# Performance work log

Hardware: AMD Instinct MI355X
Metric: run time of the kernel (lower is better)

## Reference

```python
import jax, jax.numpy as jnp
import numpy as np

E, C = 50000, 128  # edges, out_channels (heads=1 so H*C == C)
EPS = 1e-5

def _ln(x, g, b):
    m = x.mean(-1, keepdims=True)
    v = x.var(-1, keepdims=True)
    return (x - m) / jnp.sqrt(v + EPS) * g + b

def _mlp(x, W1, b1, W2, b2):
    return jax.nn.silu(x @ W1 + b1) @ W2 + b2

def setup_inputs() -> dict:
    key = jax.random.key(0)
    ks = jax.random.split(key, 32)
    s = 0.02
    d = {}
    d['edge'] = jax.random.normal(ks[0], (E, C), jnp.float32)
    d['edge_nei_len'] = jax.random.normal(ks[1], (E, 3, C), jnp.float32)
    d['edge_nei_angle'] = jax.random.normal(ks[2], (E, 3, C), jnp.float32)
    # lin_query / lin_key / lin_value (C -> H*C == C)
    d['Wq'] = jax.random.normal(ks[3], (C, C), jnp.float32) * s
    d['bq'] = jnp.zeros((C,), jnp.float32)
    d['Wk'] = jax.random.normal(ks[4], (C, C), jnp.float32) * s
    d['bk'] = jnp.zeros((C,), jnp.float32)
    d['Wv'] = jax.random.normal(ks[5], (C, C), jnp.float32) * s
    d['bv'] = jnp.zeros((C,), jnp.float32)
    # lin_key_e1/e2/e3 and lin_value_e1/e2/e3 stacked along first axis (3 lattice dirs)
    d['Wke'] = jax.random.normal(ks[6], (3, C, C), jnp.float32) * s
    d['bke'] = jnp.zeros((3, C), jnp.float32)
    d['Wve'] = jax.random.normal(ks[7], (3, C, C), jnp.float32) * s
    d['bve'] = jnp.zeros((3, C), jnp.float32)
    # lin_edge (no bias)
    d['We'] = jax.random.normal(ks[8], (C, C), jnp.float32) * s
    # lin_concate
    d['Wc'] = jax.random.normal(ks[9], (C, C), jnp.float32) * s
    d['bc'] = jnp.zeros((C,), jnp.float32)
    # key_update MLP: 3C -> C -> C
    d['Wk1'] = jax.random.normal(ks[10], (3 * C, C), jnp.float32) * s
    d['bk1'] = jnp.zeros((C,), jnp.float32)
    d['Wk2'] = jax.random.normal(ks[11], (C, C), jnp.float32) * s
    d['bk2'] = jnp.zeros((C,), jnp.float32)
    # lin_msg_update MLP: 3C -> C -> C
    d['Wm1'] = jax.random.normal(ks[12], (3 * C, C), jnp.float32) * s
    d['bm1'] = jnp.zeros((C,), jnp.float32)
    d['Wm2'] = jax.random.normal(ks[13], (C, C), jnp.float32) * s
    d['bm2'] = jnp.zeros((C,), jnp.float32)
    # LayerNorms
    d['g_att'] = jnp.ones((C,), jnp.float32)
    d['b_att'] = jnp.zeros((C,), jnp.float32)
    d['g_bn'] = jnp.ones((C,), jnp.float32)
    d['b_bn'] = jnp.zeros((C,), jnp.float32)
    return d

def reference(edge, edge_nei_len, edge_nei_angle,
              Wq, bq, Wk, bk, Wv, bv,
              Wke, bke, Wve, bve, We, Wc, bc,
              Wk1, bk1, Wk2, bk2, Wm1, bm1, Wm2, bm2,
              g_att, b_att, g_bn, b_bn):
    # per-edge projections, broadcast over the 3 lattice directions (repeat in torch)
    q = (edge @ Wq + bq)[:, None, :]           # [E,1,C]
    kx = (edge @ Wk + bk)[:, None, :]          # [E,1,C]
    vx = (edge @ Wv + bv)[:, None, :]          # [E,1,C]
    kx3 = jnp.broadcast_to(kx, (edge.shape[0], 3, kx.shape[-1]))
    vx3 = jnp.broadcast_to(vx, (edge.shape[0], 3, vx.shape[-1]))
    # per-direction projections of lattice embedding (lin_key_e1..3 / lin_value_e1..3)
    ky = jnp.einsum('eti,tio->eto', edge_nei_len, Wke) + bke   # [E,3,C]
    vy = jnp.einsum('eti,tio->eto', edge_nei_len, Wve) + bve   # [E,3,C]
    exy = edge_nei_angle @ We                                   # [E,3,C]
    # key_update MLP and attention score
    k = _mlp(jnp.concatenate([kx3, ky, exy], axis=-1), Wk1, bk1, Wk2, bk2)  # [E,3,C]
    alpha = q * k / jnp.sqrt(jnp.float32(k.shape[-1]))
    # message MLP, sigmoid gate on LayerNorm'd alpha
    msg = _mlp(jnp.concatenate([vx3, vy, exy], axis=-1), Wm1, bm1, Wm2, bm2)
    out = msg * jax.nn.sigmoid(_ln(alpha, g_att, b_att))
    out = out @ Wc + bc        # lin_concate (H*C -> C)
    out = out.sum(axis=1)      # sum over 3 directions -> [E,C]
    return jax.nn.softplus(edge + _ln(out, g_bn, b_bn))
```

## Files before the change

kernel.cpp:

```cpp
#include <hip/hip_runtime.h>

#define E_TOTAL 50000
#define NTILES  3125

#define OFF_WSB 458752ull
#define OFF_Q   524288ull
#define OFF_EK  (OFF_Q  + 12800000ull)
#define OFF_EM  (OFF_EK + 12800000ull)
#define OFF_SK  (OFF_EM + 12800000ull)
#define OFF_SM  (OFF_SK + 38400000ull)
#define OFF_P2  (OFF_SM + 38400000ull)
#define WS_NEED (OFF_P2 + 12800000ull)

typedef float f4  __attribute__((ext_vector_type(4)));
typedef short s8v __attribute__((ext_vector_type(8)));
typedef short s4v __attribute__((ext_vector_type(4)));

typedef __attribute__((address_space(3))) unsigned lds_u32;
typedef __attribute__((address_space(1))) const unsigned g_u32;

__device__ __forceinline__ short f2bf(float x){
  unsigned u = __builtin_bit_cast(unsigned, x);
  u += 0x7fffu + ((u >> 16) & 1u);
  return (short)(u >> 16);
}
__device__ __forceinline__ float bf2f(short s){
  unsigned u = ((unsigned)(unsigned short)s) << 16;
  return __builtin_bit_cast(float, u);
}
__device__ __forceinline__ float sigm(float x){ return 1.f/(1.f + __expf(-x)); }

__device__ __forceinline__ s8v load_bfrag(const float* p){
  f4 a = *(const f4*)p;
  f4 b = *(const f4*)(p + 4);
  s8v r;
  r[0]=f2bf(a[0]); r[1]=f2bf(a[1]); r[2]=f2bf(a[2]); r[3]=f2bf(a[3]);
  r[4]=f2bf(b[0]); r[5]=f2bf(b[1]); r[6]=f2bf(b[2]); r[7]=f2bf(b[3]);
  return r;
}

__device__ __forceinline__ void mm8l(f4* acc, const s8v* B, const s8v* A, int lane){
  #pragma unroll
  for (int mb = 0; mb < 8; ++mb){
    #pragma unroll
    for (int kk = 0; kk < 4; ++kk){
      s8v af = A[(mb*4 + kk)*64 + lane];
      acc[mb] = __builtin_amdgcn_mfma_f32_16x16x32_bf16(af, B[kk], acc[mb], 0, 0, 0);
    }
  }
}

__device__ __forceinline__ void mm8f(f4* acc, const s8v* B, const s8v* A, int lane){
  #pragma unroll
  for (int mb = 0; mb < 8; mb += 2){
    #pragma unroll
    for (int m2 = 0; m2 < 2; ++m2){
      #pragma unroll
      for (int kk = 0; kk < 4; ++kk){
        s8v af = A[((mb+m2)*4 + kk)*64 + lane];
        acc[mb+m2] = __builtin_amdgcn_mfma_f32_16x16x32_bf16(af, B[kk], acc[mb+m2], 0, 0, 0);
      }
    }
    __builtin_amdgcn_sched_barrier(0);
  }
}

__device__ __forceinline__ void stage_mat(const short* __restrict__ src,
                                          short* dst, int wid, int lane){
  #pragma unroll
  for (int j = 0; j < 8; ++j){
    const short* gsrc = src + j*2048 + wid*512 + lane*8;
    short* ldst = dst + j*2048 + wid*512;
    __builtin_amdgcn_global_load_lds((g_u32*)(const void*)gsrc, (lds_u32*)(void*)ldst, 16, 0, 0);
  }
}

__device__ __forceinline__ s8v pack_pair(const f4& a0, const f4& a1){
  s8v o;
  #pragma unroll
  for (int p = 0; p < 4; ++p){ o[p] = f2bf(a0[p]); o[4+p] = f2bf(a1[p]); }
  return o;
}

__global__ __launch_bounds__(256) void pack_weights(
    const float* __restrict__ Wq, const float* __restrict__ Wk, const float* __restrict__ Wv,
    const float* __restrict__ Wke, const float* __restrict__ Wve, const float* __restrict__ We,
    const float* __restrict__ Wc, const float* __restrict__ Wk1, const float* __restrict__ Wk2,
    const float* __restrict__ Wm1, const float* __restrict__ Wm2,
    short* __restrict__ wsm)
{
  int mi   = blockIdx.x >> 6;
  int elem = ((blockIdx.x & 63) << 8) + threadIdx.x;
  int p  = elem & 7;
  int l  = (elem >> 3) & 63;
  int kk = (elem >> 9) & 3;
  int mb = elem >> 11;
  int gg = l >> 4;
  int m  = mb*16 + (l & 15);
  bool dlay = (mi == 5) || (mi == 6) || (mi == 7);
  int k = dlay ? (kk*32 + ((p < 4) ? (gg*4 + p) : (16 + gg*4 + (p - 4))))
               : (kk*32 + gg*8 + p);

  const float* X = nullptr; const float* Y = nullptr; const float* W = nullptr;
  switch (mi){
    case 0: W = Wq; break;
    case 1: X = Wk; Y = Wk1;            break;
    case 2: X = Wv; Y = Wm1;            break;
    case 3: X = We; Y = Wk1 + 256*128;  break;
    case 4: X = We; Y = Wm1 + 256*128;  break;
    case 5: W = Wk2; break;
    case 6: W = Wm2; break;
    case 7: W = Wc;  break;
    default:
      if (mi < 11){ X = Wke + (mi-8)*16384;  Y = Wk1 + 128*128; }
      else        { X = Wve + (mi-11)*16384; Y = Wm1 + 128*128; }
  }
  float v;
  if (W){
    v = W[k*128 + m];
  } else {
    v = 0.f;
    for (int j = 0; j < 128; ++j) v += X[k*128 + j] * Y[j*128 + m];
  }
  wsm[(size_t)mi*16384 + elem] = f2bf(v);
}

__global__ __launch_bounds__(128) void make_biases(
    const float* __restrict__ bk,  const float* __restrict__ bke, const float* __restrict__ bk1,
    const float* __restrict__ bv,  const float* __restrict__ bve, const float* __restrict__ bm1,
    const float* __restrict__ Wk1, const float* __restrict__ Wm1,
    float* __restrict__ wsb)
{
  int b = blockIdx.x;
  int t = b % 3;
  bool isM = b >= 3;
  int o = threadIdx.x;
  const float* W  = isM ? Wm1 : Wk1;
  const float* b0 = isM ? bv  : bk;
  const float* be = (isM ? bve : bke) + t*128;
  const float* b1 = isM ? bm1 : bk1;
  float v = b1[o];
  for (int j = 0; j < 128; ++j)
    v += b0[j]*W[j*128 + o] + be[j]*W[(128 + j)*128 + o];
  wsb[b*128 + o] = v;
}

__global__ __launch_bounds__(256) void proj(
    const float* __restrict__ edge, const float* __restrict__ bq,
    const short* __restrict__ wsm, char* __restrict__ ws)
{
  __shared__ short lds[3*16384];
  const int lane = threadIdx.x & 63;
  const int wid  = threadIdx.x >> 6;
  stage_mat(wsm + 0*16384, lds,          wid, lane);
  stage_mat(wsm + 1*16384, lds + 16384,  wid, lane);
  stage_mat(wsm + 2*16384, lds + 32768,  wid, lane);
  __syncthreads();
  const int g = lane >> 4, er = lane & 15;
  short* wq  = (short*)(ws + OFF_Q);
  short* wek = (short*)(ws + OFF_EK);
  short* wem = (short*)(ws + OFF_EM);

  #pragma unroll 1
  for (int tile = blockIdx.x*4 + wid; tile < NTILES; tile += 1024){
    const float* erow = edge + ((size_t)tile*16 + er)*128;
    s8v BE[4];
    #pragma unroll
    for (int kk = 0; kk < 4; ++kk) BE[kk] = load_bfrag(erow + kk*32 + g*8);

    f4 acc[8];
    #pragma unroll
    for (int mb = 0; mb < 8; ++mb) acc[mb] = *(const f4*)(bq + mb*16 + g*4);
    mm8f(acc, BE, (const s8v*)lds, lane);
    #pragma unroll
    for (int c = 0; c < 4; ++c)
      *(s8v*)(wq + (size_t)tile*2048 + c*512 + lane*8) = pack_pair(acc[2*c], acc[2*c+1]);

    #pragma unroll
    for (int mb = 0; mb < 8; ++mb){ f4 z = {0.f,0.f,0.f,0.f}; acc[mb] = z; }
    mm8f(acc, BE, (const s8v*)(lds + 16384), lane);
    #pragma unroll
    for (int c = 0; c < 4; ++c)
      *(s8v*)(wek + (size_t)tile*2048 + c*512 + lane*8) = pack_pair(acc[2*c], acc[2*c+1]);

    #pragma unroll
    for (int mb = 0; mb < 8; ++mb){ f4 z = {0.f,0.f,0.f,0.f}; acc[mb] = z; }
    mm8f(acc, BE, (const s8v*)(lds + 32768), lane);
    #pragma unroll
    for (int c = 0; c < 4; ++c)
      *(s8v*)(wem + (size_t)tile*2048 + c*512 + lane*8) = pack_pair(acc[2*c], acc[2*c+1]);
  }
}

__global__ __launch_bounds__(256) void hpass(
    const float* __restrict__ nlen, const float* __restrict__ nang,
    const short* __restrict__ wsm, const float* __restrict__ wsb,
    char* __restrict__ ws)
{
  __shared__ short lds[4*16384];
  const int lane = threadIdx.x & 63;
  const int wid  = threadIdx.x >> 6;
  const int t    = blockIdx.y;
  stage_mat(wsm + (size_t)(8 + t)*16384,  lds,         wid, lane);
  stage_mat(wsm + 3*16384,                lds + 16384, wid, lane);
  stage_mat(wsm + (size_t)(11 + t)*16384, lds + 32768, wid, lane);
  stage_mat(wsm + 4*16384,                lds + 49152, wid, lane);
  __syncthreads();
  const int g = lane >> 4, er = lane & 15;
  const float* biasK = wsb + t*128;
  const float* biasM = wsb + 384 + t*128;
  const short* wek = (const short*)(ws + OFF_EK);
  const short* wem = (const short*)(ws + OFF_EM);
  short* wsk  = (short*)(ws + OFF_SK + (size_t)t*12800000ull);
  short* wsm2 = (short*)(ws + OFF_SM + (size_t)t*12800000ull);

  #pragma unroll 1
  for (int tile = blockIdx.x*4 + wid; tile < NTILES; tile += 1024){
    const size_t e = (size_t)tile*16 + er;
    const float* lrow = nlen + (e*3 + t)*128;
    const float* arow = nang + (e*3 + t)*128;
    s8v BL[4], BA[4];
    #pragma unroll
    for (int kk = 0; kk < 4; ++kk){
      BL[kk] = load_bfrag(lrow + kk*32 + g*8);
      BA[kk] = load_bfrag(arow + kk*32 + g*8);
    }
    f4 acc[8];
    #pragma unroll
    for (int c = 0; c < 4; ++c){
      s8v ek8 = *(const s8v*)(wek + (size_t)tile*2048 + c*512 + lane*8);
      f4 b0 = *(const f4*)(biasK + (2*c)*16 + g*4);
      f4 b1 = *(const f4*)(biasK + (2*c+1)*16 + g*4);
      #pragma unroll
      for (int r = 0; r < 4; ++r){ b0[r] += bf2f(ek8[r]); b1[r] += bf2f(ek8[4+r]); }
      acc[2*c] = b0; acc[2*c+1] = b1;
    }
    mm8f(acc, BL, (const s8v*)lds, lane);
    mm8f(acc, BA, (const s8v*)(lds + 16384), lane);
    #pragma unroll
    for (int kk = 0; kk < 4; ++kk){
      s8v S;
      #pragma unroll
      for (int p = 0; p < 4; ++p){
        float x0 = acc[2*kk][p];   S[p]   = f2bf(x0 * sigm(x0));
        float x1 = acc[2*kk+1][p]; S[4+p] = f2bf(x1 * sigm(x1));
      }
      *(s8v*)(wsk + (size_t)tile*2048 + kk*512 + lane*8) = S;
    }
    #pragma unroll
    for (int c = 0; c < 4; ++c){
      s8v em8 = *(const s8v*)(wem + (size_t)tile*2048 + c*512 + lane*8);
      f4 b0 = *(const f4*)(biasM + (2*c)*16 + g*4);
      f4 b1 = *(const f4*)(biasM + (2*c+1)*16 + g*4);
      #pragma unroll
      for (int r = 0; r < 4; ++r){ b0[r] += bf2f(em8[r]); b1[r] += bf2f(em8[4+r]); }
      acc[2*c] = b0; acc[2*c+1] = b1;
    }
    mm8f(acc, BL, (const s8v*)(lds + 32768), lane);
    mm8f(acc, BA, (const s8v*)(lds + 49152), lane);
    #pragma unroll
    for (int kk = 0; kk < 4; ++kk){
      s8v S;
      #pragma unroll
      for (int p = 0; p < 4; ++p){
        float x0 = acc[2*kk][p];   S[p]   = f2bf(x0 * sigm(x0));
        float x1 = acc[2*kk+1][p]; S[4+p] = f2bf(x1 * sigm(x1));
      }
      *(s8v*)(wsm2 + (size_t)tile*2048 + kk*512 + lane*8) = S;
    }
  }
}

__global__ __launch_bounds__(256) void gpass(
    const float* __restrict__ bk2,  const float* __restrict__ bm2,
    const float* __restrict__ g_att, const float* __restrict__ b_att,
    const short* __restrict__ wsm, char* __restrict__ ws)
{
  __shared__ short lds[2*16384];
  const int lane = threadIdx.x & 63;
  const int wid  = threadIdx.x >> 6;
  const int t    = blockIdx.y;
  stage_mat(wsm + 5*16384, lds,         wid, lane);
  stage_mat(wsm + 6*16384, lds + 16384, wid, lane);
  __syncthreads();
  const int g = lane >> 4;
  const short* wq  = (const short*)(ws + OFF_Q);
  const short* wsk = (const short*)(ws + OFF_SK + (size_t)t*12800000ull);
  const short* wsm2= (const short*)(ws + OFF_SM + (size_t)t*12800000ull);
  const size_t poff[3] = {OFF_EK, OFF_EM, OFF_P2};
  short* wp = (short*)(ws + poff[t]);

  #pragma unroll 1
  for (int tile = blockIdx.x*4 + wid; tile < NTILES; tile += 1024){
    s8v SF[4];
    #pragma unroll
    for (int kk = 0; kk < 4; ++kk)
      SF[kk] = *(const s8v*)(wsk + (size_t)tile*2048 + kk*512 + lane*8);
    f4 acc[8];
    #pragma unroll
    for (int mb = 0; mb < 8; ++mb) acc[mb] = *(const f4*)(bk2 + mb*16 + g*4);
    mm8f(acc, SF, (const s8v*)lds, lane);

    float sm = 0.f, ssq = 0.f;
    #pragma unroll
    for (int c = 0; c < 4; ++c){
      s8v q8 = *(const s8v*)(wq + (size_t)tile*2048 + c*512 + lane*8);
      #pragma unroll
      for (int r = 0; r < 4; ++r){
        float a = bf2f(q8[r])   * acc[2*c][r]   * 0.08838834764831845f;
        float b = bf2f(q8[4+r]) * acc[2*c+1][r] * 0.08838834764831845f;
        acc[2*c][r] = a; acc[2*c+1][r] = b;
        sm += a + b; ssq += a*a + b*b;
      }
    }
    sm  += __shfl_xor(sm, 16);  sm  += __shfl_xor(sm, 32);
    ssq += __shfl_xor(ssq, 16); ssq += __shfl_xor(ssq, 32);
    float mean = sm * (1.f/128.f);
    float rstd = rsqrtf(ssq * (1.f/128.f) - mean*mean + 1e-5f);
    s4v gateb[8];
    #pragma unroll
    for (int mb = 0; mb < 8; ++mb){
      f4 ga = *(const f4*)(g_att + mb*16 + g*4);
      f4 bb = *(const f4*)(b_att + mb*16 + g*4);
      s4v t4;
      #pragma unroll
      for (int r = 0; r < 4; ++r)
        t4[r] = f2bf(sigm((acc[mb][r] - mean)*rstd*ga[r] + bb[r]));
      gateb[mb] = t4;
    }

    #pragma unroll
    for (int kk = 0; kk < 4; ++kk)
      SF[kk] = *(const s8v*)(wsm2 + (size_t)tile*2048 + kk*512 + lane*8);
    #pragma unroll
    for (int mb = 0; mb < 8; ++mb) acc[mb] = *(const f4*)(bm2 + mb*16 + g*4);
    mm8f(acc, SF, (const s8v*)(lds + 16384), lane);
    #pragma unroll
    for (int c = 0; c < 4; ++c){
      s8v o;
      #pragma unroll
      for (int p = 0; p < 4; ++p){
        o[p]   = f2bf(acc[2*c][p]   * bf2f(gateb[2*c][p]));
        o[4+p] = f2bf(acc[2*c+1][p] * bf2f(gateb[2*c+1][p]));
      }
      *(s8v*)(wp + (size_t)tile*2048 + c*512 + lane*8) = o;
    }
  }
}

__global__ __launch_bounds__(256) void fin(
    const float* __restrict__ edge, const float* __restrict__ bc,
    const float* __restrict__ g_bn, const float* __restrict__ b_bn,
    const short* __restrict__ wsm, const char* __restrict__ ws,
    float* __restrict__ out)
{
  __shared__ short lds[16384];
  const int lane = threadIdx.x & 63;
  const int wid  = threadIdx.x >> 6;
  stage_mat(wsm + 7*16384, lds, wid, lane);
  __syncthreads();
  const int g = lane >> 4, er = lane & 15;
  const short* p0 = (const short*)(ws + OFF_EK);
  const short* p1 = (const short*)(ws + OFF_EM);
  const short* p2 = (const short*)(ws + OFF_P2);

  #pragma unroll 1
  for (int tile = blockIdx.x*4 + wid; tile < NTILES; tile += 784){
    const size_t e = (size_t)tile*16 + er;
    const float* erow = edge + e*128;

    s8v GF[4];
    #pragma unroll
    for (int c = 0; c < 4; ++c){
      size_t idx = (size_t)tile*2048 + c*512 + lane*8;
      s8v a = *(const s8v*)(p0 + idx);
      s8v b = *(const s8v*)(p1 + idx);
      s8v d = *(const s8v*)(p2 + idx);
      s8v o;
      #pragma unroll
      for (int i = 0; i < 8; ++i) o[i] = f2bf(bf2f(a[i]) + bf2f(b[i]) + bf2f(d[i]));
      GF[c] = o;
    }
    f4 acc[8];
    #pragma unroll
    for (int mb = 0; mb < 8; ++mb){
      f4 b = *(const f4*)(bc + mb*16 + g*4);
      #pragma unroll
      for (int r = 0; r < 4; ++r) b[r] *= 3.f;
      acc[mb] = b;
    }
    mm8f(acc, GF, (const s8v*)lds, lane);

    float sm = 0.f, ssq = 0.f;
    #pragma unroll
    for (int mb = 0; mb < 8; ++mb){
      #pragma unroll
      for (int r = 0; r < 4; ++r){ sm += acc[mb][r]; ssq += acc[mb][r]*acc[mb][r]; }
    }
    sm  += __shfl_xor(sm, 16);  sm  += __shfl_xor(sm, 32);
    ssq += __shfl_xor(ssq, 16); ssq += __shfl_xor(ssq, 32);
    float mean = sm * (1.f/128.f);
    float rstd = rsqrtf(ssq * (1.f/128.f) - mean*mean + 1e-5f);

    #pragma unroll
    for (int mb = 0; mb < 8; ++mb){
      f4 ev  = *(const f4*)(erow + mb*16 + g*4);
      f4 gv  = *(const f4*)(g_bn + mb*16 + g*4);
      f4 bv2 = *(const f4*)(b_bn + mb*16 + g*4);
      f4 o;
      #pragma unroll
      for (int r = 0; r < 4; ++r){
        float x = ev[r] + (acc[mb][r] - mean)*rstd*gv[r] + bv2[r];
        o[r] = (x > 20.f) ? x : __logf(1.f + __expf(x));
      }
      *(f4*)(out + e*128 + mb*16 + g*4) = o;
    }
  }
}

__global__ __launch_bounds__(256) void edge_fused(
    const float* __restrict__ edge, const float* __restrict__ nlen, const float* __restrict__ nang,
    const float* __restrict__ bq,   const float* __restrict__ bk2,  const float* __restrict__ bm2,
    const float* __restrict__ bc,
    const float* __restrict__ g_att, const float* __restrict__ b_att,
    const float* __restrict__ g_bn,  const float* __restrict__ b_bn,
    const short* __restrict__ wsm,  const float* __restrict__ wsb,
    float* __restrict__ out)
{
  __shared__ short smem[2*16384];
  const int lane = threadIdx.x & 63;
  const int wid  = threadIdx.x >> 6;
  int tile = blockIdx.x*4 + wid;
  if (tile > NTILES-1) tile = NTILES-1;
  const int g  = lane >> 4;
  const int er = lane & 15;
  const size_t e = (size_t)tile*16 + er;
  const float* erow = edge + e*128;

  stage_mat(wsm + 0*16384, smem, wid, lane);
  s8v BE[4];
  #pragma unroll
  for (int kk = 0; kk < 4; ++kk) BE[kk] = load_bfrag(erow + kk*32 + g*8);
  f4 acc[8], gm[8];
  s4v qb[8], ekb[8], emb[8], gateb[8];
  s8v S[4], BL[4], BA[4];
  #pragma unroll
  for (int mb = 0; mb < 8; ++mb){ f4 z = {0.f,0.f,0.f,0.f}; gm[mb] = z; }
  __syncthreads();

  stage_mat(wsm + 1*16384, smem + 16384, wid, lane);
  #pragma unroll
  for (int mb = 0; mb < 8; ++mb) acc[mb] = *(const f4*)(bq + mb*16 + g*4);
  mm8l(acc, BE, (const s8v*)smem, lane);
  #pragma unroll
  for (int mb = 0; mb < 8; ++mb){
    s4v t4; t4[0]=f2bf(acc[mb][0]); t4[1]=f2bf(acc[mb][1]); t4[2]=f2bf(acc[mb][2]); t4[3]=f2bf(acc[mb][3]);
    qb[mb] = t4;
  }
  __syncthreads();

  stage_mat(wsm + 2*16384, smem, wid, lane);
  #pragma unroll
  for (int mb = 0; mb < 8; ++mb){ f4 z = {0.f,0.f,0.f,0.f}; acc[mb] = z; }
  mm8l(acc, BE, (const s8v*)(smem + 16384), lane);
  #pragma unroll
  for (int mb = 0; mb < 8; ++mb){
    s4v t4; t4[0]=f2bf(acc[mb][0]); t4[1]=f2bf(acc[mb][1]); t4[2]=f2bf(acc[mb][2]); t4[3]=f2bf(acc[mb][3]);
    ekb[mb] = t4;
  }
  __syncthreads();

  stage_mat(wsm + 8*16384, smem + 16384, wid, lane);
  #pragma unroll
  for (int mb = 0; mb < 8; ++mb){ f4 z = {0.f,0.f,0.f,0.f}; acc[mb] = z; }
  mm8l(acc, BE, (const s8v*)smem, lane);
  #pragma unroll
  for (int mb = 0; mb < 8; ++mb){
    s4v t4; t4[0]=f2bf(acc[mb][0]); t4[1]=f2bf(acc[mb][1]); t4[2]=f2bf(acc[mb][2]); t4[3]=f2bf(acc[mb][3]);
    emb[mb] = t4;
  }
  {
    const float* lrow = nlen + e*3*128;
    const float* arow = nang + e*3*128;
    #pragma unroll
    for (int kk = 0; kk < 4; ++kk){
      BL[kk] = load_bfrag(lrow + kk*32 + g*8);
      BA[kk] = load_bfrag(arow + kk*32 + g*8);
    }
  }
  __syncthreads();

  int cur = 1;
  #pragma unroll 1
  for (int t = 0; t < 3; ++t){
    stage_mat(wsm + 3*16384, smem + (cur^1)*16384, wid, lane);
    #pragma unroll
    for (int mb = 0; mb < 8; ++mb){
      f4 b = *(const f4*)(wsb + t*128 + mb*16 + g*4);
      #pragma unroll
      for (int r = 0; r < 4; ++r) b[r] += bf2f(ekb[mb][r]);
      acc[mb] = b;
    }
    mm8l(acc, BL, (const s8v*)(smem + cur*16384), lane);
    __syncthreads(); cur ^= 1;

    stage_mat(wsm + 5*16384, smem + (cur^1)*16384, wid, lane);
    mm8l(acc, BA, (const s8v*)(smem + cur*16384), lane);
    #pragma unroll
    for (int kk = 0; kk < 4; ++kk){
      #pragma unroll
      for (int p = 0; p < 4; ++p){
        float x0 = acc[2*kk][p];   S[kk][p]   = f2bf(x0 * sigm(x0));
        float x1 = acc[2*kk+1][p]; S[kk][4+p] = f2bf(x1 * sigm(x1));
      }
    }
    __syncthreads(); cur ^= 1;

    stage_mat(wsm + (size_t)(11+t)*16384, smem + (cur^1)*16384, wid, lane);
    #pragma unroll
    for (int mb = 0; mb < 8; ++mb) acc[mb] = *(const f4*)(bk2 + mb*16 + g*4);
    mm8l(acc, S, (const s8v*)(smem + cur*16384), lane);
    {
      float sm = 0.f, ssq = 0.f;
      #pragma unroll
      for (int mb = 0; mb < 8; ++mb){
        #pragma unroll
        for (int r = 0; r < 4; ++r){
          float a = bf2f(qb[mb][r]) * acc[mb][r] * 0.08838834764831845f;
          acc[mb][r] = a; sm += a; ssq += a*a;
        }
      }
      sm  += __shfl_xor(sm, 16);  sm  += __shfl_xor(sm, 32);
      ssq += __shfl_xor(ssq, 16); ssq += __shfl_xor(ssq, 32);
      float mean = sm * (1.f/128.f);
      float rstd = rsqrtf(ssq * (1.f/128.f) - mean*mean + 1e-5f);
      #pragma unroll
      for (int mb = 0; mb < 8; ++mb){
        f4 ga = *(const f4*)(g_att + mb*16 + g*4);
        f4 bb = *(const f4*)(b_att + mb*16 + g*4);
        s4v t4;
        #pragma unroll
        for (int r = 0; r < 4; ++r)
          t4[r] = f2bf(sigm((acc[mb][r] - mean)*rstd*ga[r] + bb[r]));
        gateb[mb] = t4;
      }
    }
    __syncthreads(); cur ^= 1;

    stage_mat(wsm + 4*16384, smem + (cur^1)*16384, wid, lane);
    #pragma unroll
    for (int mb = 0; mb < 8; ++mb){
      f4 b = *(const f4*)(wsb + 384 + t*128 + mb*16 + g*4);
      #pragma unroll
      for (int r = 0; r < 4; ++r) b[r] += bf2f(emb[mb][r]);
      acc[mb] = b;
    }
    mm8l(acc, BL, (const s8v*)(smem + cur*16384), lane);
    __syncthreads(); cur ^= 1;

    stage_mat(wsm + 6*16384, smem + (cur^1)*16384, wid, lane);
    mm8l(acc, BA, (const s8v*)(smem + cur*16384), lane);
    #pragma unroll
    for (int kk = 0; kk < 4; ++kk){
      #pragma unroll
      for (int p = 0; p < 4; ++p){
        float x0 = acc[2*kk][p];   S[kk][p]   = f2bf(x0 * sigm(x0));
        float x1 = acc[2*kk+1][p]; S[kk][4+p] = f2bf(x1 * sigm(x1));
      }
    }
    __syncthreads(); cur ^= 1;

    stage_mat(wsm + (size_t)(t < 2 ? 9 + t : 7)*16384, smem + (cur^1)*16384, wid, lane);
    #pragma unroll
    for (int mb = 0; mb < 8; ++mb) acc[mb] = *(const f4*)(bm2 + mb*16 + g*4);
    mm8l(acc, S, (const s8v*)(smem + cur*16384), lane);
    if (t < 2){
      const float* lrow = nlen + (e*3 + t + 1)*128;
      const float* arow = nang + (e*3 + t + 1)*128;
      #pragma unroll
      for (int kk = 0; kk < 4; ++kk){
        BL[kk] = load_bfrag(lrow + kk*32 + g*8);
        BA[kk] = load_bfrag(arow + kk*32 + g*8);
      }
    }
    #pragma unroll
    for (int mb = 0; mb < 8; ++mb){
      #pragma unroll
      for (int r = 0; r < 4; ++r) gm[mb][r] += acc[mb][r] * bf2f(gateb[mb][r]);
    }
    __syncthreads(); cur ^= 1;
  }

  s8v GF[4];
  #pragma unroll
  for (int kk = 0; kk < 4; ++kk){
    #pragma unroll
    for (int p = 0; p < 4; ++p){
      GF[kk][p]   = f2bf(gm[2*kk][p]);
      GF[kk][4+p] = f2bf(gm[2*kk+1][p]);
    }
  }
  #pragma unroll
  for (int mb = 0; mb < 8; ++mb){
    f4 b = *(const f4*)(bc + mb*16 + g*4);
    #pragma unroll
    for (int r = 0; r < 4; ++r) b[r] *= 3.f;
    acc[mb] = b;
  }
  mm8l(acc, GF, (const s8v*)(smem + cur*16384), lane);

  float sm = 0.f, ssq = 0.f;
  #pragma unroll
  for (int mb = 0; mb < 8; ++mb){
    #pragma unroll
    for (int r = 0; r < 4; ++r){ sm += acc[mb][r]; ssq += acc[mb][r]*acc[mb][r]; }
  }
  sm  += __shfl_xor(sm, 16);  sm  += __shfl_xor(sm, 32);
  ssq += __shfl_xor(ssq, 16); ssq += __shfl_xor(ssq, 32);
  float mean = sm * (1.f/128.f);
  float rstd = rsqrtf(ssq * (1.f/128.f) - mean*mean + 1e-5f);

  #pragma unroll
  for (int mb = 0; mb < 8; ++mb){
    f4 ev  = *(const f4*)(erow + mb*16 + g*4);
    f4 gv  = *(const f4*)(g_bn + mb*16 + g*4);
    f4 bv2 = *(const f4*)(b_bn + mb*16 + g*4);
    f4 o;
    #pragma unroll
    for (int r = 0; r < 4; ++r){
      float x = ev[r] + (acc[mb][r] - mean)*rstd*gv[r] + bv2[r];
      o[r] = (x > 20.f) ? x : log1pf(__expf(x));
    }
    *(f4*)(out + e*128 + mb*16 + g*4) = o;
  }
}

extern "C" void kernel_launch(void* const* d_in, const int* in_sizes, int n_in,
                              void* d_out, int out_size, void* d_ws, size_t ws_size,
                              hipStream_t stream)
{
  const float* edge = (const float*)d_in[0];
  const float* nlen = (const float*)d_in[1];
  const float* nang = (const float*)d_in[2];
  const float* Wq  = (const float*)d_in[3];
  const float* bq  = (const float*)d_in[4];
  const float* Wk  = (const float*)d_in[5];
  const float* bk  = (const float*)d_in[6];
  const float* Wv  = (const float*)d_in[7];
  const float* bv  = (const float*)d_in[8];
  const float* Wke = (const float*)d_in[9];
  const float* bke = (const float*)d_in[10];
  const float* Wve = (const float*)d_in[11];
  const float* bve = (const float*)d_in[12];
  const float* We  = (const float*)d_in[13];
  const float* Wc  = (const float*)d_in[14];
  const float* bc  = (const float*)d_in[15];
  const float* Wk1 = (const float*)d_in[16];
  const float* bk1 = (const float*)d_in[17];
  const float* Wk2 = (const float*)d_in[18];
  const float* bk2 = (const float*)d_in[19];
  const float* Wm1 = (const float*)d_in[20];
  const float* bm1 = (const float*)d_in[21];
  const float* Wm2 = (const float*)d_in[22];
  const float* bm2 = (const float*)d_in[23];
  const float* g_att = (const float*)d_in[24];
  const float* b_att = (const float*)d_in[25];
  const float* g_bn  = (const float*)d_in[26];
  const float* b_bn  = (const float*)d_in[27];

  short* wsm = (short*)d_ws;
  float* wsb = (float*)((char*)d_ws + OFF_WSB);
  char*  ws  = (char*)d_ws;

  pack_weights<<<dim3(14*64), dim3(256), 0, stream>>>(
      Wq, Wk, Wv, Wke, Wve, We, Wc, Wk1, Wk2, Wm1, Wm2, wsm);
  make_biases<<<dim3(6), dim3(128), 0, stream>>>(
      bk, bke, bk1, bv, bve, bm1, Wk1, Wm1, wsb);

  if (ws_size >= WS_NEED){
    proj<<<dim3(256), dim3(256), 0, stream>>>(edge, bq, wsm, ws);
    hpass<<<dim3(256, 3), dim3(256), 0, stream>>>(nlen, nang, wsm, wsb, ws);
    gpass<<<dim3(256, 3), dim3(256), 0, stream>>>(bk2, bm2, g_att, b_att, wsm, ws);
    fin<<<dim3(196), dim3(256), 0, stream>>>(
        edge, bc, g_bn, b_bn, wsm, ws, (float*)d_out);
  } else {
    edge_fused<<<dim3((NTILES + 3)/4), dim3(256), 0, stream>>>(
        edge, nlen, nang, bq, bk2, bm2, bc, g_att, b_att, g_bn, b_bn,
        wsm, wsb, (float*)d_out);
  }
}
```

Baseline: 198.9 us.

## Software-pipeline neighbour-feature loads with double-buffered registers in edge MLP pass

Splits the per-tile work into an issue phase that loads the fp32 lattice length/angle rows into registers and a compute phase that converts them to bf16 and runs the MFMA MLP. The loop is unrolled by two with ping-pong register buffers, so the global loads for the next tile are in flight while the current tile computes. This hides global-memory latency at the cost of 128 extra VGPRs per thread for the two buffers, which may reduce occupancy or cause spills.

```diff
diff --git a/kernel.cpp b/kernel.cpp
--- a/kernel.cpp
+++ b/kernel.cpp
@@ -214,16 +214,32 @@
   short* wsk  = (short*)(ws + OFF_SK + (size_t)t*12800000ull);
   short* wsm2 = (short*)(ws + OFF_SM + (size_t)t*12800000ull);
 
-  #pragma unroll 1
-  for (int tile = blockIdx.x*4 + wid; tile < NTILES; tile += 1024){
+  f4 rA[16], rB[16];
+
+  auto issue = [&](int tile, f4* r){
     const size_t e = (size_t)tile*16 + er;
     const float* lrow = nlen + (e*3 + t)*128;
     const float* arow = nang + (e*3 + t)*128;
+    #pragma unroll
+    for (int kk = 0; kk < 4; ++kk){
+      r[2*kk]     = *(const f4*)(lrow + kk*32 + g*8);
+      r[2*kk+1]   = *(const f4*)(lrow + kk*32 + g*8 + 4);
+      r[8+2*kk]   = *(const f4*)(arow + kk*32 + g*8);
+      r[8+2*kk+1] = *(const f4*)(arow + kk*32 + g*8 + 4);
+    }
+  };
+
+  auto doTile = [&](int tile, const f4* r){
     s8v BL[4], BA[4];
     #pragma unroll
     for (int kk = 0; kk < 4; ++kk){
-      BL[kk] = load_bfrag(lrow + kk*32 + g*8);
-      BA[kk] = load_bfrag(arow + kk*32 + g*8);
+      s8v bl, ba;
+      #pragma unroll
+      for (int p = 0; p < 4; ++p){
+        bl[p] = f2bf(r[2*kk][p]);     bl[4+p] = f2bf(r[2*kk+1][p]);
+        ba[p] = f2bf(r[8+2*kk][p]);   ba[4+p] = f2bf(r[8+2*kk+1][p]);
+      }
+      BL[kk] = bl; BA[kk] = ba;
     }
     f4 acc[8];
     #pragma unroll
@@ -232,7 +248,7 @@
       f4 b0 = *(const f4*)(biasK + (2*c)*16 + g*4);
       f4 b1 = *(const f4*)(biasK + (2*c+1)*16 + g*4);
       #pragma unroll
-      for (int r = 0; r < 4; ++r){ b0[r] += bf2f(ek8[r]); b1[r] += bf2f(ek8[4+r]); }
+      for (int rr = 0; rr < 4; ++rr){ b0[rr] += bf2f(ek8[rr]); b1[rr] += bf2f(ek8[4+rr]); }
       acc[2*c] = b0; acc[2*c+1] = b1;
     }
     mm8f(acc, BL, (const s8v*)lds, lane);
@@ -253,7 +269,7 @@
       f4 b0 = *(const f4*)(biasM + (2*c)*16 + g*4);
       f4 b1 = *(const f4*)(biasM + (2*c+1)*16 + g*4);
       #pragma unroll
-      for (int r = 0; r < 4; ++r){ b0[r] += bf2f(em8[r]); b1[r] += bf2f(em8[4+r]); }
+      for (int rr = 0; rr < 4; ++rr){ b0[rr] += bf2f(em8[rr]); b1[rr] += bf2f(em8[4+rr]); }
       acc[2*c] = b0; acc[2*c+1] = b1;
     }
     mm8f(acc, BL, (const s8v*)(lds + 32768), lane);
@@ -268,6 +284,18 @@
       }
       *(s8v*)(wsm2 + (size_t)tile*2048 + kk*512 + lane*8) = S;
     }
+  };
+
+  const int t0 = blockIdx.x*4 + wid;
+  issue(t0, rA);
+  #pragma unroll 1
+  for (int tile = t0; tile < NTILES; tile += 2048){
+    const int tn  = tile + 1024;
+    const int tnn = tile + 2048;
+    if (tn < NTILES) issue(tn, rB);
+    doTile(tile, rA);
+    if (tnn < NTILES) issue(tnn, rA);
+    if (tn < NTILES) doTile(tn, rB);
   }
 }
 
```

Result: slower. 212.5 us (+6.8%).

## Fuse gated-message pass with final projection and loop directions in-kernel

Applied to the files above, without the earlier changes.

Merges the per-direction gating pass and the final lin_concate/LayerNorm/softplus kernel into one kernel that loops over the three directions, accumulating the gated message in fp32 registers. This removes the writes and re-reads of three bf16 intermediate buffers and one kernel launch, and drops the extra workspace region. The hpass grid is also shrunk to 85x3 blocks with a matching stride. The fused kernel carries more registers and LDS (three staged matrices), which may reduce occupancy, and the 256 blocks now cover all three directions instead of 256 per direction.

```diff
diff --git a/kernel.cpp b/kernel.cpp
--- a/kernel.cpp
+++ b/kernel.cpp
@@ -9,8 +9,7 @@
 #define OFF_EM  (OFF_EK + 12800000ull)
 #define OFF_SK  (OFF_EM + 12800000ull)
 #define OFF_SM  (OFF_SK + 38400000ull)
-#define OFF_P2  (OFF_SM + 38400000ull)
-#define WS_NEED (OFF_P2 + 12800000ull)
+#define WS_NEED (OFF_SM + 38400000ull)
 
 typedef float f4  __attribute__((ext_vector_type(4)));
 typedef short s8v __attribute__((ext_vector_type(8)));
@@ -215,7 +214,7 @@
   short* wsm2 = (short*)(ws + OFF_SM + (size_t)t*12800000ull);
 
   #pragma unroll 1
-  for (int tile = blockIdx.x*4 + wid; tile < NTILES; tile += 1024){
+  for (int tile = blockIdx.x*4 + wid; tile < NTILES; tile += 340){
     const size_t e = (size_t)tile*16 + er;
     const float* lrow = nlen + (e*3 + t)*128;
     const float* arow = nang + (e*3 + t)*128;
@@ -271,137 +270,106 @@
   }
 }
 
-__global__ __launch_bounds__(256) void gpass(
+__global__ __launch_bounds__(256) void gfin(
+    const float* __restrict__ edge,
     const float* __restrict__ bk2,  const float* __restrict__ bm2,
+    const float* __restrict__ bc,
     const float* __restrict__ g_att, const float* __restrict__ b_att,
-    const short* __restrict__ wsm, char* __restrict__ ws)
+    const float* __restrict__ g_bn,  const float* __restrict__ b_bn,
+    const short* __restrict__ wsm, const char* __restrict__ ws,
+    float* __restrict__ out)
 {
-  __shared__ short lds[2*16384];
+  __shared__ short lds[3*16384];
   const int lane = threadIdx.x & 63;
   const int wid  = threadIdx.x >> 6;
-  const int t    = blockIdx.y;
   stage_mat(wsm + 5*16384, lds,         wid, lane);
   stage_mat(wsm + 6*16384, lds + 16384, wid, lane);
+  stage_mat(wsm + 7*16384, lds + 32768, wid, lane);
   __syncthreads();
-  const int g = lane >> 4;
-  const short* wq  = (const short*)(ws + OFF_Q);
-  const short* wsk = (const short*)(ws + OFF_SK + (size_t)t*12800000ull);
-  const short* wsm2= (const short*)(ws + OFF_SM + (size_t)t*12800000ull);
-  const size_t poff[3] = {OFF_EK, OFF_EM, OFF_P2};
-  short* wp = (short*)(ws + poff[t]);
+  const int g = lane >> 4, er = lane & 15;
+  const short* wq = (const short*)(ws + OFF_Q);
 
   #pragma unroll 1
   for (int tile = blockIdx.x*4 + wid; tile < NTILES; tile += 1024){
-    s8v SF[4];
-    #pragma unroll
-    for (int kk = 0; kk < 4; ++kk)
-      SF[kk] = *(const s8v*)(wsk + (size_t)tile*2048 + kk*512 + lane*8);
-    f4 acc[8];
-    #pragma unroll
-    for (int mb = 0; mb < 8; ++mb) acc[mb] = *(const f4*)(bk2 + mb*16 + g*4);
-    mm8f(acc, SF, (const s8v*)lds, lane);
+    const size_t e = (size_t)tile*16 + er;
+    f4 gm[8], acc[8], gate[8];
+    #pragma unroll
+    for (int mb = 0; mb < 8; ++mb){ f4 z = {0.f,0.f,0.f,0.f}; gm[mb] = z; }
+
+    #pragma unroll 1
+    for (int t = 0; t < 3; ++t){
+      const short* wsk  = (const short*)(ws + OFF_SK + (size_t)t*12800000ull);
+      const short* wsm2 = (const short*)(ws + OFF_SM + (size_t)t*12800000ull);
+      s8v SF[4];
+      #pragma unroll
+      for (int kk = 0; kk < 4; ++kk)
+        SF[kk] = *(const s8v*)(wsk + (size_t)tile*2048 + kk*512 + lane*8);
+      #pragma unroll
+      for (int mb = 0; mb < 8; ++mb) acc[mb] = *(const f4*)(bk2 + mb*16 + g*4);
+      mm8f(acc, SF, (const s8v*)lds, lane);
+
+      float sm = 0.f, ssq = 0.f;
+      #pragma unroll
+      for (int c = 0; c < 4; ++c){
+        s8v q8 = *(const s8v*)(wq + (size_t)tile*2048 + c*512 + lane*8);
+        #pragma unroll
+        for (int r = 0; r < 4; ++r){
+          float a = bf2f(q8[r])   * acc[2*c][r]   * 0.08838834764831845f;
+          float b = bf2f(q8[4+r]) * acc[2*c+1][r] * 0.08838834764831845f;
+          acc[2*c][r] = a; acc[2*c+1][r] = b;
+          sm += a + b; ssq += a*a + b*b;
+        }
+      }
+      sm  += __shfl_xor(sm, 16);  sm  += __shfl_xor(sm, 32);
+      ssq += __shfl_xor(ssq, 16); ssq += __shfl_xor(ssq, 32);
+      float mean = sm * (1.f/128.f);
+      float rstd = rsqrtf(ssq * (1.f/128.f) - mean*mean + 1e-5f);
+      #pragma unroll
+      for (int mb = 0; mb < 8; ++mb){
+        f4 ga = *(const f4*)(g_att + mb*16 + g*4);
+        f4 bb = *(const f4*)(b_att + mb*16 + g*4);
+        #pragma unroll
+        for (int r = 0; r < 4; ++r)
+          gate[mb][r] = sigm((acc[mb][r] - mean)*rstd*ga[r] + bb[r]);
+      }
+
+      #pragma unroll
+      for (int kk = 0; kk < 4; ++kk)
+        SF[kk] = *(const s8v*)(wsm2 + (size_t)tile*2048 + kk*512 + lane*8);
+      #pragma unroll
+      for (int mb = 0; mb < 8; ++mb) acc[mb] = *(const f4*)(bm2 + mb*16 + g*4);
+      mm8f(acc, SF, (const s8v*)(lds + 16384), lane);
+      #pragma unroll
+      for (int mb = 0; mb < 8; ++mb){
+        #pragma unroll
+        for (int r = 0; r < 4; ++r) gm[mb][r] += acc[mb][r] * gate[mb][r];
+      }
+    }
+
+    s8v GF[4];
+    #pragma unroll
+    for (int c = 0; c < 4; ++c) GF[c] = pack_pair(gm[2*c], gm[2*c+1]);
+    #pragma unroll
+    for (int mb = 0; mb < 8; ++mb){
+      f4 b = *(const f4*)(bc + mb*16 + g*4);
+      #pragma unroll
+      for (int r = 0; r < 4; ++r) b[r] *= 3.f;
+      acc[mb] = b;
+    }
+    mm8f(acc, GF, (const s8v*)(lds + 32768), lane);
 
     float sm = 0.f, ssq = 0.f;
     #pragma unroll
-    for (int c = 0; c < 4; ++c){
-      s8v q8 = *(const s8v*)(wq + (size_t)tile*2048 + c*512 + lane*8);
-      #pragma unroll
-      for (int r = 0; r < 4; ++r){
-        float a = bf2f(q8[r])   * acc[2*c][r]   * 0.08838834764831845f;
-        float b = bf2f(q8[4+r]) * acc[2*c+1][r] * 0.08838834764831845f;
-        acc[2*c][r] = a; acc[2*c+1][r] = b;
-        sm += a + b; ssq += a*a + b*b;
-      }
+    for (int mb = 0; mb < 8; ++mb){
+      #pragma unroll
+      for (int r = 0; r < 4; ++r){ sm += acc[mb][r]; ssq += acc[mb][r]*acc[mb][r]; }
     }
     sm  += __shfl_xor(sm, 16);  sm  += __shfl_xor(sm, 32);
     ssq += __shfl_xor(ssq, 16); ssq += __shfl_xor(ssq, 32);
     float mean = sm * (1.f/128.f);
     float rstd = rsqrtf(ssq * (1.f/128.f) - mean*mean + 1e-5f);
-    s4v gateb[8];
-    #pragma unroll
-    for (int mb = 0; mb < 8; ++mb){
-      f4 ga = *(const f4*)(g_att + mb*16 + g*4);
-      f4 bb = *(const f4*)(b_att + mb*16 + g*4);
-      s4v t4;
-      #pragma unroll
-      for (int r = 0; r < 4; ++r)
-        t4[r] = f2bf(sigm((acc[mb][r] - mean)*rstd*ga[r] + bb[r]));
-      gateb[mb] = t4;
-    }
-
-    #pragma unroll
-    for (int kk = 0; kk < 4; ++kk)
-      SF[kk] = *(const s8v*)(wsm2 + (size_t)tile*2048 + kk*512 + lane*8);
-    #pragma unroll
-    for (int mb = 0; mb < 8; ++mb) acc[mb] = *(const f4*)(bm2 + mb*16 + g*4);
-    mm8f(acc, SF, (const s8v*)(lds + 16384), lane);
-    #pragma unroll
-    for (int c = 0; c < 4; ++c){
-      s8v o;
-      #pragma unroll
-      for (int p = 0; p < 4; ++p){
-        o[p]   = f2bf(acc[2*c][p]   * bf2f(gateb[2*c][p]));
-        o[4+p] = f2bf(acc[2*c+1][p] * bf2f(gateb[2*c+1][p]));
-      }
-      *(s8v*)(wp + (size_t)tile*2048 + c*512 + lane*8) = o;
-    }
-  }
-}
-
-__global__ __launch_bounds__(256) void fin(
-    const float* __restrict__ edge, const float* __restrict__ bc,
-    const float* __restrict__ g_bn, const float* __restrict__ b_bn,
-    const short* __restrict__ wsm, const char* __restrict__ ws,
-    float* __restrict__ out)
-{
-  __shared__ short lds[16384];
-  const int lane = threadIdx.x & 63;
-  const int wid  = threadIdx.x >> 6;
-  stage_mat(wsm + 7*16384, lds, wid, lane);
-  __syncthreads();
-  const int g = lane >> 4, er = lane & 15;
-  const short* p0 = (const short*)(ws + OFF_EK);
-  const short* p1 = (const short*)(ws + OFF_EM);
-  const short* p2 = (const short*)(ws + OFF_P2);
-
-  #pragma unroll 1
-  for (int tile = blockIdx.x*4 + wid; tile < NTILES; tile += 784){
-    const size_t e = (size_t)tile*16 + er;
+
     const float* erow = edge + e*128;
-
-    s8v GF[4];
-    #pragma unroll
-    for (int c = 0; c < 4; ++c){
-      size_t idx = (size_t)tile*2048 + c*512 + lane*8;
-      s8v a = *(const s8v*)(p0 + idx);
-      s8v b = *(const s8v*)(p1 + idx);
-      s8v d = *(const s8v*)(p2 + idx);
-      s8v o;
-      #pragma unroll
-      for (int i = 0; i < 8; ++i) o[i] = f2bf(bf2f(a[i]) + bf2f(b[i]) + bf2f(d[i]));
-      GF[c] = o;
-    }
-    f4 acc[8];
-    #pragma unroll
-    for (int mb = 0; mb < 8; ++mb){
-      f4 b = *(const f4*)(bc + mb*16 + g*4);
-      #pragma unroll
-      for (int r = 0; r < 4; ++r) b[r] *= 3.f;
-      acc[mb] = b;
-    }
-    mm8f(acc, GF, (const s8v*)lds, lane);
-
-    float sm = 0.f, ssq = 0.f;
-    #pragma unroll
-    for (int mb = 0; mb < 8; ++mb){
-      #pragma unroll
-      for (int r = 0; r < 4; ++r){ sm += acc[mb][r]; ssq += acc[mb][r]*acc[mb][r]; }
-    }
-    sm  += __shfl_xor(sm, 16);  sm  += __shfl_xor(sm, 32);
-    ssq += __shfl_xor(ssq, 16); ssq += __shfl_xor(ssq, 32);
-    float mean = sm * (1.f/128.f);
-    float rstd = rsqrtf(ssq * (1.f/128.f) - mean*mean + 1e-5f);
-
     #pragma unroll
     for (int mb = 0; mb < 8; ++mb){
       f4 ev  = *(const f4*)(erow + mb*16 + g*4);
@@ -679,10 +647,9 @@
 
   if (ws_size >= WS_NEED){
     proj<<<dim3(256), dim3(256), 0, stream>>>(edge, bq, wsm, ws);
-    hpass<<<dim3(256, 3), dim3(256), 0, stream>>>(nlen, nang, wsm, wsb, ws);
-    gpass<<<dim3(256, 3), dim3(256), 0, stream>>>(bk2, bm2, g_att, b_att, wsm, ws);
-    fin<<<dim3(196), dim3(256), 0, stream>>>(
-        edge, bc, g_bn, b_bn, wsm, ws, (float*)d_out);
+    hpass<<<dim3(85, 3), dim3(256), 0, stream>>>(nlen, nang, wsm, wsb, ws);
+    gfin<<<dim3(256), dim3(256), 0, stream>>>(
+        edge, bk2, bm2, bc, g_att, b_att, g_bn, b_bn, wsm, ws, (float*)d_out);
   } else {
     edge_fused<<<dim3((NTILES + 3)/4), dim3(256), 0, stream>>>(
         edge, nlen, nang, bq, bk2, bm2, bc, g_att, b_att, g_bn, b_bn,
```

Measured after the change: 179.6 us (median of 2 runs). 9.7% less time.
